# Performance work log

Measured on AMD Instinct MI355X. Metric: run time of the kernel, lower is better.

The kernel has to match this reference:

```python
import jax, jax.numpy as jnp
import numpy as np

B, T, D = 2, 2048, 1024
N_HEADS = 16
HEAD_DIM = D // N_HEADS


def setup_inputs() -> dict:
    key = jax.random.key(0)
    ks = jax.random.split(key, 5)
    s = 0.02
    return {
        "x": jax.random.normal(ks[0], (B, T, D), jnp.float32),
        "wq": jax.random.normal(ks[1], (D, D), jnp.float32) * s,
        "wk": jax.random.normal(ks[2], (D, D), jnp.float32) * s,
        "wv": jax.random.normal(ks[3], (D, D), jnp.float32) * s,
        "wo": jax.random.normal(ks[4], (D, D), jnp.float32) * s,
        "bo": jnp.zeros((D,), jnp.float32),
    }


def reference(x, wq, wk, wv, wo, bo):
    b, t, _ = x.shape
    # QKV projections (weights stored [d_in, d_out]); reshape to (b, heads, t, head_dim)
    def split_heads(y):
        return y.reshape(b, t, N_HEADS, HEAD_DIM).transpose(0, 2, 1, 3)
    q = split_heads(x @ wq)
    k = split_heads(x @ wk)
    v = split_heads(x @ wv)
    # causal attention scores: (b, h, t, t)
    scores = jnp.einsum("bhqd,bhkd->bhqk", q, k)
    causal = jnp.tril(jnp.ones((t, t), bool))  # True where attending allowed
    scores = jnp.where(causal, scores, -jnp.inf)
    attn = jax.nn.softmax(scores / np.sqrt(HEAD_DIM).astype(np.float32), axis=-1)
    # dropout_rate = 0.0 (eval mode) -> identity
    ctx = jnp.einsum("bhqk,bhkd->bhqd", attn, v)
    ctx = ctx.transpose(0, 2, 1, 3).reshape(b, t, D)
    return ctx @ wo + bo
```

## Files before the change

kernel.cpp:

```cpp
#include <hip/hip_runtime.h>
#include <hip/hip_bf16.h>
#include <cstdint>

typedef __hip_bfloat16 bf16;
typedef __bf16 bf16x8 __attribute__((ext_vector_type(8)));
typedef __bf16 bf16x4 __attribute__((ext_vector_type(4)));
typedef float f32x4 __attribute__((ext_vector_type(4)));
typedef uint32_t u32x4 __attribute__((ext_vector_type(4)));

#define LOG2E 1.4426950408889634f

__device__ __forceinline__ void gload_lds16(const void* g, void* l) {
  __builtin_amdgcn_global_load_lds(
      (const __attribute__((address_space(1))) unsigned int*)g,
      (__attribute__((address_space(3))) unsigned int*)l,
      16, 0, 0);
}

__device__ __forceinline__ uint32_t pack_bf16(float a, float b) {
  const uint32_t ha = (uint32_t)__builtin_bit_cast(uint16_t, (__bf16)a);
  const uint32_t hb = (uint32_t)__builtin_bit_cast(uint16_t, (__bf16)b);
  return ha | (hb << 16);
}

__device__ __forceinline__ float softmax_pack(const f32x4 (&s8)[8], u32x4 (&paw)[4],
                                              float negsh) {
  float rsum = 0.f;
#pragma unroll
  for (int kk = 0; kk < 4; ++kk) {
    const float p0 = exp2f(fmaf(s8[2 * kk][0], LOG2E, negsh));
    const float p1 = exp2f(fmaf(s8[2 * kk][1], LOG2E, negsh));
    const float p2 = exp2f(fmaf(s8[2 * kk][2], LOG2E, negsh));
    const float p3 = exp2f(fmaf(s8[2 * kk][3], LOG2E, negsh));
    const float p4 = exp2f(fmaf(s8[2 * kk + 1][0], LOG2E, negsh));
    const float p5 = exp2f(fmaf(s8[2 * kk + 1][1], LOG2E, negsh));
    const float p6 = exp2f(fmaf(s8[2 * kk + 1][2], LOG2E, negsh));
    const float p7 = exp2f(fmaf(s8[2 * kk + 1][3], LOG2E, negsh));
    rsum += ((p0 + p1) + (p2 + p3)) + ((p4 + p5) + (p6 + p7));
    u32x4 w;
    w[0] = pack_bf16(p0, p1);
    w[1] = pack_bf16(p2, p3);
    w[2] = (uint32_t)__shfl_xor((int)pack_bf16(p4, p5), 16);
    w[3] = (uint32_t)__shfl_xor((int)pack_bf16(p6, p7), 16);
    paw[kk] = w;
  }
  return rsum;
}

__global__ void conv_k(const float* __restrict__ src, bf16* __restrict__ dst, int n) {
  const int i = (blockIdx.x * 256 + threadIdx.x) * 8;
  if (i >= n) return;
  const f32x4 a = *(const f32x4*)(src + i);
  const f32x4 b = *(const f32x4*)(src + i + 4);
  bf16x8 o;
#pragma unroll
  for (int j = 0; j < 4; ++j) { o[j] = (__bf16)a[j]; o[4 + j] = (__bf16)b[j]; }
  *(bf16x8*)(dst + i) = o;
}

__global__ void transpose_conv4(
    const float* __restrict__ wq, const float* __restrict__ wk,
    const float* __restrict__ wv, const float* __restrict__ wo,
    bf16* __restrict__ dqkv, bf16* __restrict__ dout) {
  __shared__ float tile[32][33];
  const int z = blockIdx.z;
  const float* src = (z == 0) ? wq : ((z == 1) ? wk : ((z == 2) ? wv : wo));
  bf16* dst = (z < 3) ? (dqkv + (long)z * 1048576) : dout;
  const int bx = blockIdx.x * 32, by = blockIdx.y * 32;
  const int tx = threadIdx.x;
  for (int j = threadIdx.y; j < 32; j += 8)
    tile[j][tx] = src[(long)(by + j) * 1024 + bx + tx];
  __syncthreads();
  for (int j = threadIdx.y; j < 32; j += 8)
    dst[(long)(bx + j) * 1024 + by + tx] = __float2bfloat16(tile[tx][j]);
}

__global__ __launch_bounds__(256, 2) void gemm_qkv(
    const bf16* __restrict__ A, const bf16* __restrict__ Bt,
    bf16* __restrict__ Cq, bf16* __restrict__ Ck, bf16* __restrict__ Cv,
    int M, int N, int K) {
  __shared__ __align__(16) bf16 As[128 * 64];
  __shared__ __align__(16) bf16 Bs[128 * 64];

  const int tid = threadIdx.x;
  const int lane = tid & 63;
  const int wave = tid >> 6;
  const int quad = lane >> 4;
  const int l16 = lane & 15;
  const int id = (int)blockIdx.y * 24 + (int)blockIdx.x;
  const int xcd = id & 7, idx = id >> 3;
  const int bxn = xcd * 3 + idx % 3;
  const int byn = idx / 3;
  const int m0 = byn * 128;
  const int n0 = bxn * 128;
  const int wm = (wave >> 1) * 64;
  const int wn = (wave & 1) * 64;

  const f32x4 zero4 = {0.f, 0.f, 0.f, 0.f};
  f32x4 acc[4][4];
#pragma unroll
  for (int mi = 0; mi < 4; ++mi)
#pragma unroll
    for (int ni = 0; ni < 4; ++ni) acc[mi][ni] = zero4;

  const int sRow = tid >> 3;
  const int sK = (tid & 7) * 8;
  const int sSwz = sK ^ (8 * (sRow & 7));
  const bf16* Ag = A + (long)(m0 + sRow) * K + sSwz;
  const bf16* Bg = Bt + (long)(n0 + sRow) * K + sSwz;
  const int swzr = 8 * (l16 & 7);

  for (int k0 = 0; k0 < K; k0 += 64) {
#pragma unroll
    for (int j = 0; j < 4; ++j) {
      gload_lds16(Ag + k0 + (long)(32 * j) * K, &As[tid * 8 + 2048 * j]);
      gload_lds16(Bg + k0 + (long)(32 * j) * K, &Bs[tid * 8 + 2048 * j]);
    }
    __syncthreads();

#pragma unroll
    for (int ks = 0; ks < 64; ks += 32) {
      const int colr = (ks + quad * 8) ^ swzr;
      bf16x8 af[4], bfv[4];
#pragma unroll
      for (int mi = 0; mi < 4; ++mi)
        af[mi] = *(const bf16x8*)&As[(wm + mi * 16 + l16) * 64 + colr];
#pragma unroll
      for (int ni = 0; ni < 4; ++ni)
        bfv[ni] = *(const bf16x8*)&Bs[(wn + ni * 16 + l16) * 64 + colr];
#pragma unroll
      for (int mi = 0; mi < 4; ++mi)
#pragma unroll
        for (int ni = 0; ni < 4; ++ni)
          acc[mi][ni] = __builtin_amdgcn_mfma_f32_16x16x32_bf16(af[mi], bfv[ni], acc[mi][ni], 0, 0, 0);
    }
    __syncthreads();
  }

#pragma unroll
  for (int mi = 0; mi < 4; ++mi) {
    const int gmb = m0 + wm + mi * 16 + quad * 4;
#pragma unroll
    for (int ni = 0; ni < 4; ++ni) {
      const int n = n0 + wn + ni * 16 + l16;
      const int which = n >> 10, rem = n & 1023;
      const int h = rem >> 6, hd = rem & 63;
      bf16* dst = (which == 0) ? Cq : ((which == 1) ? Ck : Cv);
#pragma unroll
      for (int r = 0; r < 4; ++r) {
        const int gm = gmb + r;
        const int b = gm >> 11, t = gm & 2047;
        dst[(((long)(b * 16 + h)) * 2048 + t) * 64 + hd] = __float2bfloat16(acc[mi][ni][r]);
      }
    }
  }
}

__global__ __launch_bounds__(256, 3) void gemm_out(
    const bf16* __restrict__ A, const bf16* __restrict__ Bt,
    const float* __restrict__ bias, float* __restrict__ Cout,
    int M, int N, int K) {
  __shared__ __align__(16) bf16 As[64 * 32];
  __shared__ __align__(16) bf16 Bs[128 * 32];

  const int tid = threadIdx.x;
  const int lane = tid & 63;
  const int wave = tid >> 6;
  const int quad = lane >> 4;
  const int l16 = lane & 15;
  const int id = (int)blockIdx.y * 8 + (int)blockIdx.x;
  const int m0 = (id >> 3) * 64;
  const int n0 = (id & 7) * 128;
  const int wm = (wave & 1) * 32;
  const int wn = (wave >> 1) * 64;

  const f32x4 zero4 = {0.f, 0.f, 0.f, 0.f};
  f32x4 acc[2][4];
#pragma unroll
  for (int mi = 0; mi < 2; ++mi)
#pragma unroll
    for (int ni = 0; ni < 4; ++ni) acc[mi][ni] = zero4;

  const int sRow = tid >> 2;
  const int sK = (tid & 3) * 8;
  const bf16* Ag = A + (long)(m0 + sRow) * K + sK;
  const bf16* Bg = Bt + (long)(n0 + sRow) * K + sK;
  const bf16* Bg2 = Bg + 64L * K;

  for (int k0 = 0; k0 < K; k0 += 32) {
    gload_lds16(Ag + k0, &As[tid * 8]);
    gload_lds16(Bg + k0, &Bs[tid * 8]);
    gload_lds16(Bg2 + k0, &Bs[tid * 8 + 2048]);
    __syncthreads();

    bf16x8 af[2], bfv[4];
#pragma unroll
    for (int mi = 0; mi < 2; ++mi)
      af[mi] = *(const bf16x8*)&As[(wm + mi * 16 + l16) * 32 + quad * 8];
#pragma unroll
    for (int ni = 0; ni < 4; ++ni)
      bfv[ni] = *(const bf16x8*)&Bs[(wn + ni * 16 + l16) * 32 + quad * 8];
#pragma unroll
    for (int mi = 0; mi < 2; ++mi)
#pragma unroll
      for (int ni = 0; ni < 4; ++ni)
        acc[mi][ni] = __builtin_amdgcn_mfma_f32_16x16x32_bf16(af[mi], bfv[ni], acc[mi][ni], 0, 0, 0);
    __syncthreads();
  }

#pragma unroll
  for (int mi = 0; mi < 2; ++mi) {
    const int gmb = m0 + wm + mi * 16 + quad * 4;
#pragma unroll
    for (int ni = 0; ni < 4; ++ni) {
      const int n = n0 + wn + ni * 16 + l16;
      const float bv = bias[n];
#pragma unroll
      for (int r = 0; r < 4; ++r)
        Cout[(long)(gmb + r) * N + n] = acc[mi][ni][r] + bv;
    }
  }
}

__global__ __launch_bounds__(256, 2) void attn_kernel(
    const bf16* __restrict__ Q, const bf16* __restrict__ Kg, const bf16* __restrict__ Vg,
    bf16* __restrict__ ctx) {
  constexpr int KSTR = 72, VSTR = 136;
  __shared__ __align__(16) bf16 Ks[128 * KSTR];
  __shared__ __align__(16) bf16 Vt[64 * VSTR];

  const int tid = threadIdx.x;
  const int lane = tid & 63;
  const int wave = tid >> 6;
  const int quad = lane >> 4;
  const int l16 = lane & 15;

  const int id = (int)blockIdx.y * 16 + (int)blockIdx.x;
  const int g = id & 7;
  const int bh = g * 4 + ((id >> 3) & 3);
  const int pp = id >> 5;
  const int tq = (pp < 8) ? pp : 23 - pp;

  const long base = (long)bh * 2048 * 64;
  const int b = bh >> 4, h = bh & 15;

  const int qbaseA = tq * 128 + wave * 16;
  const int qbaseB = qbaseA + 64;

  bf16x8 qfA0 = *(const bf16x8*)(Q + base + (long)(qbaseA + l16) * 64 + quad * 8);
  bf16x8 qfA1 = *(const bf16x8*)(Q + base + (long)(qbaseA + l16) * 64 + 32 + quad * 8);
  bf16x8 qfB0 = *(const bf16x8*)(Q + base + (long)(qbaseB + l16) * 64 + quad * 8);
  bf16x8 qfB1 = *(const bf16x8*)(Q + base + (long)(qbaseB + l16) * 64 + 32 + quad * 8);
#pragma unroll
  for (int j = 0; j < 8; ++j) {
    qfA0[j] = (__bf16)((float)qfA0[j] * 0.125f);
    qfA1[j] = (__bf16)((float)qfA1[j] * 0.125f);
    qfB0[j] = (__bf16)((float)qfB0[j] * 0.125f);
    qfB1[j] = (__bf16)((float)qfB1[j] * 0.125f);
  }

  const f32x4 zero4 = {0.f, 0.f, 0.f, 0.f};
  float l_iA = 0.f, l_iB = 0.f;
  f32x4 oaccA[4], oaccB[4];
#pragma unroll
  for (int nb = 0; nb < 4; ++nb) { oaccA[nb] = zero4; oaccB[nb] = zero4; }

  const int krow = tid >> 1;
  const int kc32 = (tid & 1) * 32;
  const int vr4 = (tid & 31) * 4;
  const int vd8 = (tid >> 5) * 8;
  const int vb4 = (vr4 >> 4) & 1;
  const int vc4 = (vr4 & ~31) + 8 * (((vr4 >> 2) & 3) ^ vb4) + 4 * vb4;

  const float negsh = -12.0f * LOG2E;

  const int nk = tq + 1;
  bf16x8 kr[4], vv[4];
  {
    const bf16* kp = Kg + base + (long)krow * 64 + kc32;
#pragma unroll
    for (int i = 0; i < 4; ++i) kr[i] = *(const bf16x8*)(kp + i * 8);
#pragma unroll
    for (int i = 0; i < 4; ++i)
      vv[i] = *(const bf16x8*)(Vg + base + (long)(vr4 + i) * 64 + vd8);
  }

  for (int kt = 0; kt < nk; ++kt) {
    const int k0 = kt * 128;
#pragma unroll
    for (int i = 0; i < 4; ++i)
      *(bf16x8*)&Ks[krow * KSTR + kc32 + i * 8] = kr[i];
#pragma unroll
    for (int j = 0; j < 8; ++j) {
      bf16x4 t;
      t[0] = vv[0][j]; t[1] = vv[1][j]; t[2] = vv[2][j]; t[3] = vv[3][j];
      *(bf16x4*)&Vt[(vd8 + j) * VSTR + vc4] = t;
    }
    __syncthreads();
    if (kt + 1 < nk) {
      const bf16* kp = Kg + base + (long)(k0 + 128 + krow) * 64 + kc32;
#pragma unroll
      for (int i = 0; i < 4; ++i) kr[i] = *(const bf16x8*)(kp + i * 8);
#pragma unroll
      for (int i = 0; i < 4; ++i)
        vv[i] = *(const bf16x8*)(Vg + base + (long)(k0 + 128 + vr4 + i) * 64 + vd8);
    }

    f32x4 sA[8], sB[8];
    __builtin_amdgcn_s_setprio(1);
#pragma unroll
    for (int kb = 0; kb < 8; ++kb) {
      const bf16x8 kb0 = *(const bf16x8*)&Ks[(kb * 16 + l16) * KSTR + quad * 8];
      const bf16x8 kb1 = *(const bf16x8*)&Ks[(kb * 16 + l16) * KSTR + 32 + quad * 8];
      f32x4 aA = zero4, aB = zero4;
      aA = __builtin_amdgcn_mfma_f32_16x16x32_bf16(kb0, qfA0, aA, 0, 0, 0);
      aB = __builtin_amdgcn_mfma_f32_16x16x32_bf16(kb0, qfB0, aB, 0, 0, 0);
      aA = __builtin_amdgcn_mfma_f32_16x16x32_bf16(kb1, qfA1, aA, 0, 0, 0);
      aB = __builtin_amdgcn_mfma_f32_16x16x32_bf16(kb1, qfB1, aB, 0, 0, 0);
      sA[kb] = aA; sB[kb] = aB;
    }
    __builtin_amdgcn_s_setprio(0);

    if (kt == nk - 1) {
      const int qgA = wave * 16 + l16 - quad * 4;
      const int qgB = qgA + 64;
#pragma unroll
      for (int kb = 0; kb < 8; ++kb)
#pragma unroll
        for (int r = 0; r < 4; ++r) {
          sA[kb][r] = (kb * 16 + r <= qgA) ? sA[kb][r] : -1e30f;
          sB[kb][r] = (kb * 16 + r <= qgB) ? sB[kb][r] : -1e30f;
        }
    }

    u32x4 pawA[4], pawB[4];
    float rsumA = softmax_pack(sA, pawA, negsh);
    float rsumB = softmax_pack(sB, pawB, negsh);

    __builtin_amdgcn_s_setprio(1);
#pragma unroll
    for (int kk = 0; kk < 4; ++kk) {
      const bf16x8 paA = __builtin_bit_cast(bf16x8, pawA[kk]);
      const bf16x8 paB = __builtin_bit_cast(bf16x8, pawB[kk]);
#pragma unroll
      for (int nb2 = 0; nb2 < 4; ++nb2) {
        const bf16x8 vb = *(const bf16x8*)&Vt[(nb2 * 16 + l16) * VSTR + kk * 32 + quad * 8];
        oaccA[nb2] = __builtin_amdgcn_mfma_f32_16x16x32_bf16(paA, vb, oaccA[nb2], 0, 0, 0);
        oaccB[nb2] = __builtin_amdgcn_mfma_f32_16x16x32_bf16(paB, vb, oaccB[nb2], 0, 0, 0);
      }
    }
    __builtin_amdgcn_s_setprio(0);

    rsumA += __shfl_xor(rsumA, 16);
    rsumA += __shfl_xor(rsumA, 32);
    l_iA += rsumA;
    rsumB += __shfl_xor(rsumB, 16);
    rsumB += __shfl_xor(rsumB, 32);
    l_iB += rsumB;
    __syncthreads();
  }

  {
    float linv[4];
#pragma unroll
    for (int r = 0; r < 4; ++r) linv[r] = 1.0f / __shfl(l_iA, quad * 4 + r);
#pragma unroll
    for (int r = 0; r < 4; ++r) {
      const int t = qbaseA + quad * 4 + r;
#pragma unroll
      for (int nb2 = 0; nb2 < 4; ++nb2) {
        const int d = h * 64 + nb2 * 16 + l16;
        ctx[((long)b * 2048 + t) * 1024 + d] = __float2bfloat16(oaccA[nb2][r] * linv[r]);
      }
    }
  }
  {
    float linv[4];
#pragma unroll
    for (int r = 0; r < 4; ++r) linv[r] = 1.0f / __shfl(l_iB, quad * 4 + r);
#pragma unroll
    for (int r = 0; r < 4; ++r) {
      const int t = qbaseB + quad * 4 + r;
#pragma unroll
      for (int nb2 = 0; nb2 < 4; ++nb2) {
        const int d = h * 64 + nb2 * 16 + l16;
        ctx[((long)b * 2048 + t) * 1024 + d] = __float2bfloat16(oaccB[nb2][r] * linv[r]);
      }
    }
  }
}

extern "C" void kernel_launch(void* const* d_in, const int* in_sizes, int n_in,
                              void* d_out, int out_size, void* d_ws, size_t ws_size,
                              hipStream_t stream) {
  const float* x  = (const float*)d_in[0];
  const float* wq = (const float*)d_in[1];
  const float* wk = (const float*)d_in[2];
  const float* wv = (const float*)d_in[3];
  const float* wo = (const float*)d_in[4];
  const float* bo = (const float*)d_in[5];
  float* out = (float*)d_out;

  bf16* Wtqkv = (bf16*)d_ws;
  bf16* Wto   = Wtqkv + 3145728;
  bf16* xb    = Wto + 1048576;
  bf16* Qb    = xb + 4194304;
  bf16* Kb    = Qb + 4194304;
  bf16* Vb    = Kb + 4194304;
  bf16* Cx    = xb;

  hipLaunchKernelGGL(conv_k, dim3(2048), dim3(256), 0, stream, x, xb, 4194304);
  hipLaunchKernelGGL(transpose_conv4, dim3(32, 32, 4), dim3(32, 8), 0, stream,
                     wq, wk, wv, wo, Wtqkv, Wto);

  hipLaunchKernelGGL(gemm_qkv, dim3(24, 32), dim3(256), 0, stream,
                     xb, Wtqkv, Qb, Kb, Vb, 4096, 3072, 1024);

  hipLaunchKernelGGL(attn_kernel, dim3(16, 32), dim3(256), 0, stream, Qb, Kb, Vb, Cx);

  hipLaunchKernelGGL(gemm_out, dim3(8, 64), dim3(256), 0, stream,
                     Cx, Wto, bo, out, 4096, 1024, 1024);
}
```

Measured before the change: 188.5 us.

## Split attention KV range across wave pairs and widen out-proj GEMM K-tile with swizzle

The attention kernel now has each block handle two 64-row query tiles, paired so causal work balances. The two wave pairs each process alternating 128-key blocks from a doubled K/V shared buffer, and their partial outputs and row sums are reduced through shared memory at the end. The output projection GEMM now loads a 64-wide K slice per iteration with an XOR-swizzled LDS layout, which halves the barriers and is meant to reduce bank conflicts. The costs are more LDS per block, an extra cross-wave reduction step, and possible idle wave pairs when the number of key blocks is odd.

```diff
diff --git a/kernel.cpp b/kernel.cpp
--- a/kernel.cpp
+++ b/kernel.cpp
@@ -160,8 +160,8 @@
     const bf16* __restrict__ A, const bf16* __restrict__ Bt,
     const float* __restrict__ bias, float* __restrict__ Cout,
     int M, int N, int K) {
-  __shared__ __align__(16) bf16 As[64 * 32];
-  __shared__ __align__(16) bf16 Bs[128 * 32];
+  __shared__ __align__(16) bf16 As[64 * 64];
+  __shared__ __align__(16) bf16 Bs[128 * 64];
 
   const int tid = threadIdx.x;
   const int lane = tid & 63;
@@ -181,30 +181,38 @@
 #pragma unroll
     for (int ni = 0; ni < 4; ++ni) acc[mi][ni] = zero4;
 
-  const int sRow = tid >> 2;
-  const int sK = (tid & 3) * 8;
-  const bf16* Ag = A + (long)(m0 + sRow) * K + sK;
-  const bf16* Bg = Bt + (long)(n0 + sRow) * K + sK;
-  const bf16* Bg2 = Bg + 64L * K;
-
-  for (int k0 = 0; k0 < K; k0 += 32) {
-    gload_lds16(Ag + k0, &As[tid * 8]);
-    gload_lds16(Bg + k0, &Bs[tid * 8]);
-    gload_lds16(Bg2 + k0, &Bs[tid * 8 + 2048]);
-    __syncthreads();
-
-    bf16x8 af[2], bfv[4];
-#pragma unroll
-    for (int mi = 0; mi < 2; ++mi)
-      af[mi] = *(const bf16x8*)&As[(wm + mi * 16 + l16) * 32 + quad * 8];
-#pragma unroll
-    for (int ni = 0; ni < 4; ++ni)
-      bfv[ni] = *(const bf16x8*)&Bs[(wn + ni * 16 + l16) * 32 + quad * 8];
-#pragma unroll
-    for (int mi = 0; mi < 2; ++mi)
+  const int sRow = tid >> 3;
+  const int sK = (tid & 7) * 8;
+  const int sSwz = sK ^ (8 * (sRow & 7));
+  const bf16* Ag = A + (long)(m0 + sRow) * K + sSwz;
+  const bf16* Bg = Bt + (long)(n0 + sRow) * K + sSwz;
+  const int swzr = 8 * (l16 & 7);
+
+  for (int k0 = 0; k0 < K; k0 += 64) {
+#pragma unroll
+    for (int j = 0; j < 2; ++j)
+      gload_lds16(Ag + k0 + (long)(32 * j) * K, &As[tid * 8 + 2048 * j]);
+#pragma unroll
+    for (int j = 0; j < 4; ++j)
+      gload_lds16(Bg + k0 + (long)(32 * j) * K, &Bs[tid * 8 + 2048 * j]);
+    __syncthreads();
+
+#pragma unroll
+    for (int ks = 0; ks < 64; ks += 32) {
+      const int colr = (ks + quad * 8) ^ swzr;
+      bf16x8 af[2], bfv[4];
+#pragma unroll
+      for (int mi = 0; mi < 2; ++mi)
+        af[mi] = *(const bf16x8*)&As[(wm + mi * 16 + l16) * 64 + colr];
 #pragma unroll
       for (int ni = 0; ni < 4; ++ni)
-        acc[mi][ni] = __builtin_amdgcn_mfma_f32_16x16x32_bf16(af[mi], bfv[ni], acc[mi][ni], 0, 0, 0);
+        bfv[ni] = *(const bf16x8*)&Bs[(wn + ni * 16 + l16) * 64 + colr];
+#pragma unroll
+      for (int mi = 0; mi < 2; ++mi)
+#pragma unroll
+        for (int ni = 0; ni < 4; ++ni)
+          acc[mi][ni] = __builtin_amdgcn_mfma_f32_16x16x32_bf16(af[mi], bfv[ni], acc[mi][ni], 0, 0, 0);
+    }
     __syncthreads();
   }
 
@@ -226,44 +234,24 @@
     const bf16* __restrict__ Q, const bf16* __restrict__ Kg, const bf16* __restrict__ Vg,
     bf16* __restrict__ ctx) {
   constexpr int KSTR = 72, VSTR = 136;
-  __shared__ __align__(16) bf16 Ks[128 * KSTR];
-  __shared__ __align__(16) bf16 Vt[64 * VSTR];
+  __shared__ __align__(16) bf16 Ks[256 * KSTR];
+  __shared__ __align__(16) bf16 Vt[2][64 * VSTR];
 
   const int tid = threadIdx.x;
   const int lane = tid & 63;
   const int wave = tid >> 6;
   const int quad = lane >> 4;
   const int l16 = lane & 15;
+  const int wp = wave >> 1;
+  const int wl = wave & 1;
 
   const int id = (int)blockIdx.y * 16 + (int)blockIdx.x;
   const int g = id & 7;
   const int bh = g * 4 + ((id >> 3) & 3);
-  const int pp = id >> 5;
-  const int tq = (pp < 8) ? pp : 23 - pp;
+  const int p = id >> 5;
 
   const long base = (long)bh * 2048 * 64;
   const int b = bh >> 4, h = bh & 15;
-
-  const int qbaseA = tq * 128 + wave * 16;
-  const int qbaseB = qbaseA + 64;
-
-  bf16x8 qfA0 = *(const bf16x8*)(Q + base + (long)(qbaseA + l16) * 64 + quad * 8);
-  bf16x8 qfA1 = *(const bf16x8*)(Q + base + (long)(qbaseA + l16) * 64 + 32 + quad * 8);
-  bf16x8 qfB0 = *(const bf16x8*)(Q + base + (long)(qbaseB + l16) * 64 + quad * 8);
-  bf16x8 qfB1 = *(const bf16x8*)(Q + base + (long)(qbaseB + l16) * 64 + 32 + quad * 8);
-#pragma unroll
-  for (int j = 0; j < 8; ++j) {
-    qfA0[j] = (__bf16)((float)qfA0[j] * 0.125f);
-    qfA1[j] = (__bf16)((float)qfA1[j] * 0.125f);
-    qfB0[j] = (__bf16)((float)qfB0[j] * 0.125f);
-    qfB1[j] = (__bf16)((float)qfB1[j] * 0.125f);
-  }
-
-  const f32x4 zero4 = {0.f, 0.f, 0.f, 0.f};
-  float l_iA = 0.f, l_iB = 0.f;
-  f32x4 oaccA[4], oaccB[4];
-#pragma unroll
-  for (int nb = 0; nb < 4; ++nb) { oaccA[nb] = zero4; oaccB[nb] = zero4; }
 
   const int krow = tid >> 1;
   const int kc32 = (tid & 1) * 32;
@@ -273,120 +261,183 @@
   const int vc4 = (vr4 & ~31) + 8 * (((vr4 >> 2) & 3) ^ vb4) + 4 * vb4;
 
   const float negsh = -12.0f * LOG2E;
-
-  const int nk = tq + 1;
-  bf16x8 kr[4], vv[4];
-  {
-    const bf16* kp = Kg + base + (long)krow * 64 + kc32;
-#pragma unroll
-    for (int i = 0; i < 4; ++i) kr[i] = *(const bf16x8*)(kp + i * 8);
-#pragma unroll
-    for (int i = 0; i < 4; ++i)
-      vv[i] = *(const bf16x8*)(Vg + base + (long)(vr4 + i) * 64 + vd8);
-  }
-
-  for (int kt = 0; kt < nk; ++kt) {
-    const int k0 = kt * 128;
-#pragma unroll
-    for (int i = 0; i < 4; ++i)
-      *(bf16x8*)&Ks[krow * KSTR + kc32 + i * 8] = kr[i];
+  const f32x4 zero4 = {0.f, 0.f, 0.f, 0.f};
+
+#pragma unroll 1
+  for (int seg = 0; seg < 2; ++seg) {
+    const int qt = seg ? (31 - p) : p;
+    const int qbase = qt * 64;
+    const int qrA = qbase + wl * 16 + l16;
+
+    bf16x8 qfA0 = *(const bf16x8*)(Q + base + (long)qrA * 64 + quad * 8);
+    bf16x8 qfA1 = *(const bf16x8*)(Q + base + (long)qrA * 64 + 32 + quad * 8);
+    bf16x8 qfB0 = *(const bf16x8*)(Q + base + (long)(qrA + 32) * 64 + quad * 8);
+    bf16x8 qfB1 = *(const bf16x8*)(Q + base + (long)(qrA + 32) * 64 + 32 + quad * 8);
 #pragma unroll
     for (int j = 0; j < 8; ++j) {
-      bf16x4 t;
-      t[0] = vv[0][j]; t[1] = vv[1][j]; t[2] = vv[2][j]; t[3] = vv[3][j];
-      *(bf16x4*)&Vt[(vd8 + j) * VSTR + vc4] = t;
-    }
-    __syncthreads();
-    if (kt + 1 < nk) {
-      const bf16* kp = Kg + base + (long)(k0 + 128 + krow) * 64 + kc32;
-#pragma unroll
-      for (int i = 0; i < 4; ++i) kr[i] = *(const bf16x8*)(kp + i * 8);
+      qfA0[j] = (__bf16)((float)qfA0[j] * 0.125f);
+      qfA1[j] = (__bf16)((float)qfA1[j] * 0.125f);
+      qfB0[j] = (__bf16)((float)qfB0[j] * 0.125f);
+      qfB1[j] = (__bf16)((float)qfB1[j] * 0.125f);
+    }
+
+    float l_iA = 0.f, l_iB = 0.f;
+    f32x4 oaccA[4], oaccB[4];
+#pragma unroll
+    for (int nb = 0; nb < 4; ++nb) { oaccA[nb] = zero4; oaccB[nb] = zero4; }
+
+    const int nk = (qt + 2) >> 1;
+    const int nit = (nk + 1) >> 1;
+
+    bf16x8 kr0[4], kr1[4], vv0[4], vv1[4];
+    {
+      const bf16* kp = Kg + base + (long)krow * 64 + kc32;
+#pragma unroll
+      for (int i = 0; i < 4; ++i) kr0[i] = *(const bf16x8*)(kp + i * 8);
+#pragma unroll
+      for (int i = 0; i < 4; ++i) kr1[i] = *(const bf16x8*)(kp + 128 * 64 + i * 8);
 #pragma unroll
       for (int i = 0; i < 4; ++i)
-        vv[i] = *(const bf16x8*)(Vg + base + (long)(k0 + 128 + vr4 + i) * 64 + vd8);
-    }
-
-    f32x4 sA[8], sB[8];
-    __builtin_amdgcn_s_setprio(1);
-#pragma unroll
-    for (int kb = 0; kb < 8; ++kb) {
-      const bf16x8 kb0 = *(const bf16x8*)&Ks[(kb * 16 + l16) * KSTR + quad * 8];
-      const bf16x8 kb1 = *(const bf16x8*)&Ks[(kb * 16 + l16) * KSTR + 32 + quad * 8];
-      f32x4 aA = zero4, aB = zero4;
-      aA = __builtin_amdgcn_mfma_f32_16x16x32_bf16(kb0, qfA0, aA, 0, 0, 0);
-      aB = __builtin_amdgcn_mfma_f32_16x16x32_bf16(kb0, qfB0, aB, 0, 0, 0);
-      aA = __builtin_amdgcn_mfma_f32_16x16x32_bf16(kb1, qfA1, aA, 0, 0, 0);
-      aB = __builtin_amdgcn_mfma_f32_16x16x32_bf16(kb1, qfB1, aB, 0, 0, 0);
-      sA[kb] = aA; sB[kb] = aB;
-    }
-    __builtin_amdgcn_s_setprio(0);
-
-    if (kt == nk - 1) {
-      const int qgA = wave * 16 + l16 - quad * 4;
-      const int qgB = qgA + 64;
-#pragma unroll
-      for (int kb = 0; kb < 8; ++kb)
+        vv0[i] = *(const bf16x8*)(Vg + base + (long)(vr4 + i) * 64 + vd8);
+#pragma unroll
+      for (int i = 0; i < 4; ++i)
+        vv1[i] = *(const bf16x8*)(Vg + base + (long)(128 + vr4 + i) * 64 + vd8);
+    }
+
+    for (int it = 0; it < nit; ++it) {
+#pragma unroll
+      for (int i = 0; i < 4; ++i)
+        *(bf16x8*)&Ks[krow * KSTR + kc32 + i * 8] = kr0[i];
+#pragma unroll
+      for (int i = 0; i < 4; ++i)
+        *(bf16x8*)&Ks[(128 + krow) * KSTR + kc32 + i * 8] = kr1[i];
+#pragma unroll
+      for (int j = 0; j < 8; ++j) {
+        bf16x4 t0, t1;
+        t0[0] = vv0[0][j]; t0[1] = vv0[1][j]; t0[2] = vv0[2][j]; t0[3] = vv0[3][j];
+        t1[0] = vv1[0][j]; t1[1] = vv1[1][j]; t1[2] = vv1[2][j]; t1[3] = vv1[3][j];
+        *(bf16x4*)&Vt[0][(vd8 + j) * VSTR + vc4] = t0;
+        *(bf16x4*)&Vt[1][(vd8 + j) * VSTR + vc4] = t1;
+      }
+      __syncthreads();
+
+      if (it + 1 < nit) {
+        const long knext = (long)(it * 256 + 256);
+        const bf16* kp = Kg + base + (knext + krow) * 64 + kc32;
+#pragma unroll
+        for (int i = 0; i < 4; ++i) kr0[i] = *(const bf16x8*)(kp + i * 8);
+#pragma unroll
+        for (int i = 0; i < 4; ++i) kr1[i] = *(const bf16x8*)(kp + 128 * 64 + i * 8);
+#pragma unroll
+        for (int i = 0; i < 4; ++i)
+          vv0[i] = *(const bf16x8*)(Vg + base + (knext + vr4 + i) * 64 + vd8);
+#pragma unroll
+        for (int i = 0; i < 4; ++i)
+          vv1[i] = *(const bf16x8*)(Vg + base + (knext + 128 + vr4 + i) * 64 + vd8);
+      }
+
+      const int myk = 2 * it + wp;
+      if (myk < nk) {
+        const int k0 = myk * 128;
+        const bf16* ksw = &Ks[(wp * 128) * KSTR];
+
+        f32x4 sA[8], sB[8];
+        __builtin_amdgcn_s_setprio(1);
+#pragma unroll
+        for (int kb = 0; kb < 8; ++kb) {
+          const bf16x8 kb0 = *(const bf16x8*)&ksw[(kb * 16 + l16) * KSTR + quad * 8];
+          const bf16x8 kb1 = *(const bf16x8*)&ksw[(kb * 16 + l16) * KSTR + 32 + quad * 8];
+          f32x4 aA = zero4, aB = zero4;
+          aA = __builtin_amdgcn_mfma_f32_16x16x32_bf16(kb0, qfA0, aA, 0, 0, 0);
+          aB = __builtin_amdgcn_mfma_f32_16x16x32_bf16(kb0, qfB0, aB, 0, 0, 0);
+          aA = __builtin_amdgcn_mfma_f32_16x16x32_bf16(kb1, qfA1, aA, 0, 0, 0);
+          aB = __builtin_amdgcn_mfma_f32_16x16x32_bf16(kb1, qfB1, aB, 0, 0, 0);
+          sA[kb] = aA; sB[kb] = aB;
+        }
+        __builtin_amdgcn_s_setprio(0);
+
+        if (myk == nk - 1) {
+          const int qgA = qrA - k0 - quad * 4;
+          const int qgB = qgA + 32;
+#pragma unroll
+          for (int kb = 0; kb < 8; ++kb)
+#pragma unroll
+            for (int r = 0; r < 4; ++r) {
+              sA[kb][r] = (kb * 16 + r <= qgA) ? sA[kb][r] : -1e30f;
+              sB[kb][r] = (kb * 16 + r <= qgB) ? sB[kb][r] : -1e30f;
+            }
+        }
+
+        u32x4 pawA[4], pawB[4];
+        float rsumA = softmax_pack(sA, pawA, negsh);
+        float rsumB = softmax_pack(sB, pawB, negsh);
+
+        __builtin_amdgcn_s_setprio(1);
+#pragma unroll
+        for (int kk = 0; kk < 4; ++kk) {
+          const bf16x8 paA = __builtin_bit_cast(bf16x8, pawA[kk]);
+          const bf16x8 paB = __builtin_bit_cast(bf16x8, pawB[kk]);
+#pragma unroll
+          for (int nb2 = 0; nb2 < 4; ++nb2) {
+            const bf16x8 vb = *(const bf16x8*)&Vt[wp][(nb2 * 16 + l16) * VSTR + kk * 32 + quad * 8];
+            oaccA[nb2] = __builtin_amdgcn_mfma_f32_16x16x32_bf16(paA, vb, oaccA[nb2], 0, 0, 0);
+            oaccB[nb2] = __builtin_amdgcn_mfma_f32_16x16x32_bf16(paB, vb, oaccB[nb2], 0, 0, 0);
+          }
+        }
+        __builtin_amdgcn_s_setprio(0);
+
+        rsumA += __shfl_xor(rsumA, 16);
+        rsumA += __shfl_xor(rsumA, 32);
+        l_iA += rsumA;
+        rsumB += __shfl_xor(rsumB, 16);
+        rsumB += __shfl_xor(rsumB, 32);
+        l_iB += rsumB;
+      }
+      __syncthreads();
+    }
+
+    float* scr = (float*)&Ks[0];
+    if (wp == 1) {
+      float* s = scr + (wl * 64 + lane) * 36;
+#pragma unroll
+      for (int nb = 0; nb < 4; ++nb)
 #pragma unroll
         for (int r = 0; r < 4; ++r) {
-          sA[kb][r] = (kb * 16 + r <= qgA) ? sA[kb][r] : -1e30f;
-          sB[kb][r] = (kb * 16 + r <= qgB) ? sB[kb][r] : -1e30f;
-        }
-    }
-
-    u32x4 pawA[4], pawB[4];
-    float rsumA = softmax_pack(sA, pawA, negsh);
-    float rsumB = softmax_pack(sB, pawB, negsh);
-
-    __builtin_amdgcn_s_setprio(1);
-#pragma unroll
-    for (int kk = 0; kk < 4; ++kk) {
-      const bf16x8 paA = __builtin_bit_cast(bf16x8, pawA[kk]);
-      const bf16x8 paB = __builtin_bit_cast(bf16x8, pawB[kk]);
-#pragma unroll
-      for (int nb2 = 0; nb2 < 4; ++nb2) {
-        const bf16x8 vb = *(const bf16x8*)&Vt[(nb2 * 16 + l16) * VSTR + kk * 32 + quad * 8];
-        oaccA[nb2] = __builtin_amdgcn_mfma_f32_16x16x32_bf16(paA, vb, oaccA[nb2], 0, 0, 0);
-        oaccB[nb2] = __builtin_amdgcn_mfma_f32_16x16x32_bf16(paB, vb, oaccB[nb2], 0, 0, 0);
-      }
-    }
-    __builtin_amdgcn_s_setprio(0);
-
-    rsumA += __shfl_xor(rsumA, 16);
-    rsumA += __shfl_xor(rsumA, 32);
-    l_iA += rsumA;
-    rsumB += __shfl_xor(rsumB, 16);
-    rsumB += __shfl_xor(rsumB, 32);
-    l_iB += rsumB;
-    __syncthreads();
-  }
-
-  {
-    float linv[4];
-#pragma unroll
-    for (int r = 0; r < 4; ++r) linv[r] = 1.0f / __shfl(l_iA, quad * 4 + r);
-#pragma unroll
-    for (int r = 0; r < 4; ++r) {
-      const int t = qbaseA + quad * 4 + r;
-#pragma unroll
-      for (int nb2 = 0; nb2 < 4; ++nb2) {
-        const int d = h * 64 + nb2 * 16 + l16;
-        ctx[((long)b * 2048 + t) * 1024 + d] = __float2bfloat16(oaccA[nb2][r] * linv[r]);
-      }
-    }
-  }
-  {
-    float linv[4];
-#pragma unroll
-    for (int r = 0; r < 4; ++r) linv[r] = 1.0f / __shfl(l_iB, quad * 4 + r);
-#pragma unroll
-    for (int r = 0; r < 4; ++r) {
-      const int t = qbaseB + quad * 4 + r;
-#pragma unroll
-      for (int nb2 = 0; nb2 < 4; ++nb2) {
-        const int d = h * 64 + nb2 * 16 + l16;
-        ctx[((long)b * 2048 + t) * 1024 + d] = __float2bfloat16(oaccB[nb2][r] * linv[r]);
-      }
-    }
+          s[nb * 4 + r] = oaccA[nb][r];
+          s[16 + nb * 4 + r] = oaccB[nb][r];
+        }
+      s[32] = l_iA; s[33] = l_iB;
+    }
+    __syncthreads();
+    if (wp == 0) {
+      const float* s = scr + (wl * 64 + lane) * 36;
+#pragma unroll
+      for (int nb = 0; nb < 4; ++nb)
+#pragma unroll
+        for (int r = 0; r < 4; ++r) {
+          oaccA[nb][r] += s[nb * 4 + r];
+          oaccB[nb][r] += s[16 + nb * 4 + r];
+        }
+      l_iA += s[32]; l_iB += s[33];
+
+      float linvA[4], linvB[4];
+#pragma unroll
+      for (int r = 0; r < 4; ++r) {
+        linvA[r] = 1.0f / __shfl(l_iA, quad * 4 + r);
+        linvB[r] = 1.0f / __shfl(l_iB, quad * 4 + r);
+      }
+#pragma unroll
+      for (int r = 0; r < 4; ++r) {
+        const int tA = qbase + wl * 16 + quad * 4 + r;
+#pragma unroll
+        for (int nb2 = 0; nb2 < 4; ++nb2) {
+          const int d = h * 64 + nb2 * 16 + l16;
+          ctx[((long)b * 2048 + tA) * 1024 + d] = __float2bfloat16(oaccA[nb2][r] * linvA[r]);
+          ctx[((long)b * 2048 + tA + 32) * 1024 + d] = __float2bfloat16(oaccB[nb2][r] * linvB[r]);
+        }
+      }
+    }
+    __syncthreads();
   }
 }
 
```

Result: slower. 205.5 us (+9.0%).
